# Kernel tuning notes

Measured on AMD Instinct MI355X. Metric: run time of the kernel, lower is better.

## Reference

```python
import jax, jax.numpy as jnp
import numpy as np

NUM_STEPS = 50   # global num_steps in source
SCALE = 1000     # global scale in source (fc1 out / fc2 in)
SUBTHRESH = 0.5  # HeavisideBoxcar surrogate half-width
THRESH = 1.0     # firing threshold

@jax.custom_vjp
def heaviside_boxcar(x):
    # spike = H(x); surrogate grad = boxcar of half-width SUBTHRESH
    return (x >= 0.0).astype(x.dtype)

def _hb_fwd(x):
    return heaviside_boxcar(x), x

def _hb_bwd(x, g):
    return (g * (jnp.abs(x) < SUBTHRESH).astype(g.dtype),)

heaviside_boxcar.defvjp(_hb_fwd, _hb_bwd)


def setup_inputs() -> dict:
    key = jax.random.key(0)
    k1, k2, k3 = jax.random.split(key, 3)
    B = 1024
    x = jax.random.uniform(k1, (B, 784), dtype=jnp.float32)  # pixel intensities in [0,1]
    W1 = jax.random.normal(k2, (SCALE, 784), jnp.float32) / np.sqrt(784).astype(np.float32)
    W2 = jax.random.normal(k3, (100, SCALE), jnp.float32) / np.sqrt(SCALE).astype(np.float32)
    tau_0 = jnp.array([2.0], jnp.float32)       # sigmoid(2) ~ 0.88 decay
    tau_vector = jnp.array([2.0], jnp.float32)
    acc_tau = jnp.array([2.0], jnp.float32)
    return {"x": x, "W1": W1, "W2": W2, "tau_0": tau_0,
            "tau_vector": tau_vector, "acc_tau": acc_tau}


def reference(x, W1, W2, tau_0, tau_vector, acc_tau):
    B = x.shape[0]
    # snn.spikegen.rate: per-step Bernoulli(p=x) spikes, shape [T, B, 784]
    u = jax.random.uniform(jax.random.key(42), (NUM_STEPS, B, 784), dtype=x.dtype)
    x_spk = (u < x[None]).astype(x.dtype)

    decay_0 = jax.nn.sigmoid(tau_0[0])
    decay_v = jax.nn.sigmoid(tau_vector[0])
    acc_decay = jax.nn.sigmoid(acc_tau[0])

    h1_mem = jnp.full((B, SCALE), 0.5, x.dtype)
    h1_spk = jnp.zeros((B, SCALE), x.dtype)
    h2_mem = jnp.full((B, 100), 0.5, x.dtype)
    h2_spk = jnp.zeros((B, 100), x.dtype)
    acc = jnp.zeros((B, 10), x.dtype)

    def step(carry, xt):
        h1m, h1s, h2m, h2s, acc = carry
        # pPLIF: mem = mem*decay*(1-spk) + I ; spike = H(mem - thresh)
        h1m = h1m * decay_0 * (1.0 - h1s) + xt @ W1.T
        h1s = heaviside_boxcar(h1m - THRESH)
        h2m = h2m * decay_v * (1.0 - h2s) + h1s @ W2.T
        h2s = heaviside_boxcar(h2m - THRESH)
        boost = jnp.mean(h2s.reshape(B, 10, 10), axis=2)  # AvgPool1d(10,10)
        acc = acc * acc_decay + boost                      # pPLI accumulator
        return (h1m, h1s, h2m, h2s, acc), None

    carry, _ = jax.lax.scan(step, (h1_mem, h1_spk, h2_mem, h2_spk, acc),
                            x_spk[:NUM_STEPS - 1])
    # torch loop runs under no_grad with detach(): block grads through it
    h1m, h1s, h2m, h2s, acc = jax.tree_util.tree_map(jax.lax.stop_gradient, carry)

    # final, differentiable step
    h1m = h1m * decay_0 * (1.0 - h1s) + x_spk[NUM_STEPS - 1] @ W1.T
    h1s = heaviside_boxcar(h1m - THRESH)
    h2m = h2m * decay_v * (1.0 - h2s) + h1s @ W2.T
    h2s = heaviside_boxcar(h2m - THRESH)
    boost = jnp.mean(h2s.reshape(B, 10, 10), axis=2)
    acc = acc * acc_decay + boost
    return acc
```

## Files before the change

kernel.cpp:

```cpp
#include <hip/hip_runtime.h>
#include <hip/hip_bf16.h>
#include <math.h>


#define NSTEPS 50
#define KC1 13
#define NSL 5
#define SYNC_EVERY 5

typedef __attribute__((ext_vector_type(4)))  int i32x4;
typedef __attribute__((ext_vector_type(16))) int i32x16;

#define OFF_B1     0ull
#define OFF_B2     4259840ull
#define OFF_AF     4915200ull
#define OFF_H1SC   47513600ull
#define OFF_T2     99942400ull
#define OFF_H2M    152371200ull
#define OFF_H2S    153419776ull
#define OFF_ACC    153550848ull
#define OFF_BAR    153632768ull
#define WS_END     153633280ull

#define PREP_BLOCKS 3840
#define SPK_BLOCKS 10400

__device__ __forceinline__ unsigned int rotl32(unsigned int v, int d) {
#if __has_builtin(__builtin_amdgcn_alignbit)
  return __builtin_amdgcn_alignbit(v, v, (unsigned int)(32 - d));
#else
  return (v << d) | (v >> (32 - d));
#endif
}

__device__ __forceinline__ unsigned int tf_bits(unsigned int i) {
  const unsigned int ks0 = 0u;
  const unsigned int ks1 = 42u;
  const unsigned int ks2 = 0x1BD11BDAu ^ 0u ^ 42u;
  unsigned int x0 = 0u + ks0;
  unsigned int x1 = i + ks1;
#define TF_RND(r) { x0 += x1; x1 = rotl32(x1, r); x1 ^= x0; }
  TF_RND(13) TF_RND(15) TF_RND(26) TF_RND(6)
  x0 += ks1; x1 += ks2 + 1u;
  TF_RND(17) TF_RND(29) TF_RND(16) TF_RND(24)
  x0 += ks2; x1 += ks0 + 2u;
  TF_RND(13) TF_RND(15) TF_RND(26) TF_RND(6)
  x0 += ks0; x1 += ks1 + 3u;
  TF_RND(17) TF_RND(29) TF_RND(16) TF_RND(24)
  x0 += ks1; x1 += ks2 + 4u;
  TF_RND(13) TF_RND(15) TF_RND(26) TF_RND(6)
  x0 += ks2; x1 += ks0 + 5u;
#undef TF_RND
  return x0 ^ x1;
}

__device__ __forceinline__ void spike_block(
    const float* __restrict__ x, i32x4* __restrict__ A, int gblk, int tid) {
  int g = gblk * 4 + (tid >> 6);
  int lane = tid & 63;
  int kc = g % 13;
  int r = g / 13;
  int mt = r & 63;
  int t = r >> 6;
  int b = mt * 16 + (lane & 15);
  int j0 = kc * 64 + ((lane >> 4) << 4);
  unsigned int wds[4] = {0u, 0u, 0u, 0u};
  if (j0 < 784) {
    unsigned int base = (unsigned int)(t * 1024 + b) * 784u + (unsigned int)j0;
    const float* xp = x + b * 784 + j0;
#pragma unroll
    for (int q = 0; q < 4; ++q) {
      float4 xv = *(const float4*)(xp + 4 * q);
      unsigned int K0 = (unsigned int)(int)ceilf(xv.x * 8388608.0f);
      unsigned int K1 = (unsigned int)(int)ceilf(xv.y * 8388608.0f);
      unsigned int K2 = (unsigned int)(int)ceilf(xv.z * 8388608.0f);
      unsigned int K3 = (unsigned int)(int)ceilf(xv.w * 8388608.0f);
      unsigned int w4 = 0u;
      if ((tf_bits(base + 4 * q + 0) >> 9) < K0) w4 |= 1u;
      if ((tf_bits(base + 4 * q + 1) >> 9) < K1) w4 |= 1u << 8;
      if ((tf_bits(base + 4 * q + 2) >> 9) < K2) w4 |= 1u << 16;
      if ((tf_bits(base + 4 * q + 3) >> 9) < K3) w4 |= 1u << 24;
      wds[q] = w4;
    }
  }
  i32x4 v;
  v.x = (int)wds[0]; v.y = (int)wds[1]; v.z = (int)wds[2]; v.w = (int)wds[3];
  A[(size_t)((t * 64 + mt) * 13 + kc) * 64 + lane] = v;
}

__global__ __launch_bounds__(256) void setup_kernel(
    const float* __restrict__ W1, const float* __restrict__ W2,
    signed char* __restrict__ B1, signed char* __restrict__ B2,
    const float* __restrict__ x, i32x4* __restrict__ A,
    unsigned int* __restrict__ bar) {
  if (blockIdx.x >= PREP_BLOCKS) {
    spike_block(x, A, blockIdx.x - PREP_BLOCKS, threadIdx.x);
    return;
  }
  if (blockIdx.x == 0 && threadIdx.x < 128) bar[threadIdx.x] = 0u;
  int idx = blockIdx.x * 256 + threadIdx.x;
  const int NB1 = 64 * 13 * 64 * 16;
  float w;
  signed char* dst;
  size_t stride;
  if (idx < NB1) {
    int jj = idx & 15;
    int lane = (idx >> 4) & 63;
    int kc = (idx >> 10) % 13;
    int nt = (idx >> 10) / 13;
    int k = kc * 64 + ((lane >> 4) << 4) + jj;
    int o = nt * 16 + (lane & 15);
    w = (o < 1000 && k < 784) ? W1[o * 784 + k] : 0.0f;
    dst = B1 + (size_t)(nt * 13 + kc) * 5120 + (lane << 4) + jj;
    stride = 1024;
  } else {
    int m2 = idx - NB1;
    int jj = m2 & 15;
    int lane = (m2 >> 4) & 63;
    int kc = (m2 >> 10) & 31;
    int nt = (m2 >> 10) >> 5;
    int k = kc * 32 + ((lane >> 5) << 4) + jj;
    int o = nt * 32 + (lane & 31);
    w = (o < 100 && k < 1000) ? W2[o * 1000 + k] : 0.0f;
    dst = B2 + (size_t)(nt * 32 + kc) * 1024 + (lane << 4) + jj;
    stride = 4 * 32 * 1024;
  }
  long long V = llrint((double)w * 281474976710656.0);
  signed char d = (signed char)(V & 0xFF);
  V = (V - (long long)d) >> 8;
#pragma unroll
  for (int s = 0; s < 5; ++s) {
    d = (signed char)(V & 0xFF);
    V = (V - (long long)d) >> 8;
    dst[(size_t)s * stride] = d;
  }
}

#define F1_EPI16(CP, mi, hpp, r) do {                                         \
    double td = (double)CP[4][r];                                             \
    td = td * 256.0 + (double)CP[3][r];                                       \
    td = td * 256.0 + (double)CP[2][r];                                       \
    td = td * 256.0 + (double)CP[1][r];                                       \
    td = td * 256.0 + (double)CP[0][r];                                       \
    double I = td * 0x1p-40;                                                  \
    double mm = (((spk >> (mi)) & 1u) ? 0.0 : m[mi] * alpha) + I;             \
    m[mi] = mm;                                                               \
    unsigned int sp = ((mm - 1.0) >= 0.0) ? 1u : 0u;                          \
    spk = (spk & ~(1u << (mi))) | (sp << (mi));                               \
    hpp[(r) * 16] = (signed char)sp;                                          \
  } while (0)

#define F1_STEP(WA, WB, EA, EB, DOEPI, LAST, PAR) do {                        \
    _Pragma("unroll")                                                         \
    for (int kc = 0; kc < 13; ++kc) {                                         \
      const int sl = (kc + (PAR)) & 1;                                        \
      i32x4 avA = aA[sl], avB = aB[sl];                                       \
      if (kc + 2 < 13) {                                                      \
        aA[sl] = AtA[(kc + 2) * 64];                                          \
        aB[sl] = AtB[(kc + 2) * 64];                                          \
      } else if (!(LAST)) {                                                   \
        aA[sl] = AtA[(kc + 2 - 13) * 64 + 53248];                             \
        aB[sl] = AtB[(kc + 2 - 13) * 64 + 53248];                             \
      }                                                                       \
      i32x4 q0 = bR[sl][0], q1 = bR[sl][1],                                   \
            q2 = bR[sl][2], q3 = bR[sl][3];                                   \
      i32x4 q4 = p4[kc];                                                      \
      if (kc + 2 < 13) {                                                      \
        _Pragma("unroll")                                                     \
        for (int s = 0; s < 4; ++s)                                           \
          bR[sl][s] = blsv[((kc + 2) * 4 + s) * 64 + lane];                   \
      } else {                                                                \
        _Pragma("unroll")                                                     \
        for (int s = 0; s < 4; ++s)                                           \
          bR[sl][s] = blsv[((kc + 2 - 13) * 4 + s) * 64 + lane];              \
      }                                                                       \
      if (kc == 0) {                                                          \
        WA[0] = __builtin_amdgcn_mfma_i32_16x16x64_i8(avA, q0, Z, 0, 0, 0);   \
        WB[0] = __builtin_amdgcn_mfma_i32_16x16x64_i8(avB, q0, Z, 0, 0, 0);   \
        WA[1] = __builtin_amdgcn_mfma_i32_16x16x64_i8(avA, q1, Z, 0, 0, 0);   \
        WB[1] = __builtin_amdgcn_mfma_i32_16x16x64_i8(avB, q1, Z, 0, 0, 0);   \
        WA[2] = __builtin_amdgcn_mfma_i32_16x16x64_i8(avA, q2, Z, 0, 0, 0);   \
        WB[2] = __builtin_amdgcn_mfma_i32_16x16x64_i8(avB, q2, Z, 0, 0, 0);   \
        WA[3] = __builtin_amdgcn_mfma_i32_16x16x64_i8(avA, q3, Z, 0, 0, 0);   \
        WB[3] = __builtin_amdgcn_mfma_i32_16x16x64_i8(avB, q3, Z, 0, 0, 0);   \
        WA[4] = __builtin_amdgcn_mfma_i32_16x16x64_i8(avA, q4, Z, 0, 0, 0);   \
        WB[4] = __builtin_amdgcn_mfma_i32_16x16x64_i8(avB, q4, Z, 0, 0, 0);   \
      } else {                                                                \
        WA[0] = __builtin_amdgcn_mfma_i32_16x16x64_i8(avA, q0, WA[0], 0,0,0); \
        WB[0] = __builtin_amdgcn_mfma_i32_16x16x64_i8(avB, q0, WB[0], 0,0,0); \
        WA[1] = __builtin_amdgcn_mfma_i32_16x16x64_i8(avA, q1, WA[1], 0,0,0); \
        WB[1] = __builtin_amdgcn_mfma_i32_16x16x64_i8(avB, q1, WB[1], 0,0,0); \
        WA[2] = __builtin_amdgcn_mfma_i32_16x16x64_i8(avA, q2, WA[2], 0,0,0); \
        WB[2] = __builtin_amdgcn_mfma_i32_16x16x64_i8(avB, q2, WB[2], 0,0,0); \
        WA[3] = __builtin_amdgcn_mfma_i32_16x16x64_i8(avA, q3, WA[3], 0,0,0); \
        WB[3] = __builtin_amdgcn_mfma_i32_16x16x64_i8(avB, q3, WB[3], 0,0,0); \
        WA[4] = __builtin_amdgcn_mfma_i32_16x16x64_i8(avA, q4, WA[4], 0,0,0); \
        WB[4] = __builtin_amdgcn_mfma_i32_16x16x64_i8(avB, q4, WB[4], 0,0,0); \
      }                                                                       \
      if ((DOEPI) && kc >= 1 && kc <= 4) F1_EPI16(EA, kc - 1, hpA, kc - 1);   \
      if ((DOEPI) && kc >= 5 && kc <= 8) F1_EPI16(EB, kc - 1, hpB, kc - 5);   \
    }                                                                         \
    if (DOEPI) { hpA += 1048576; hpB += 1048576; }                            \
    if (!(LAST)) { AtA += 53248; AtB += 53248; }                              \
  } while (0)

__global__ __launch_bounds__(512, 1) void fused1_kernel(
    const signed char* __restrict__ B1, const i32x4* __restrict__ Afc,
    signed char* __restrict__ h1sc, const float* __restrict__ tau0,
    unsigned int* __restrict__ bar) {
  extern __shared__ i32x4 blsv[];
  const int tid = threadIdx.x, lane = tid & 63, wv = tid >> 6;
  const int id = (int)blockIdx.x;
  const int mtg = id & 3, nt = id >> 2;
  const int mtA = mtg * 16 + wv * 2;
  const i32x4* B1v = (const i32x4*)B1;

  for (int r = tid; r < 3328; r += 512) {
    int kc = r >> 8;
    int rem = r & 255;
    blsv[r] = B1v[(size_t)nt * 4160 + (size_t)kc * 320 + rem];
  }

  i32x4 p4[13];
#pragma unroll
  for (int kc = 0; kc < 13; ++kc)
    p4[kc] = B1v[(size_t)nt * 4160 + (size_t)kc * 320 + 4 * 64 + lane];

  const double alpha = 1.0 / (1.0 + exp(-(double)tau0[0]));
  double m[8];
  unsigned int spk = 0;
#pragma unroll
  for (int r = 0; r < 8; ++r) m[r] = 0.5;

  i32x4 Z;
  Z.x = 0; Z.y = 0; Z.z = 0; Z.w = 0;
  i32x4 Ca[5], Cb[5];
  i32x4 Da[5], Db[5];

  const i32x4* AtA = Afc + (size_t)(mtA * 13) * 64 + lane;
  const i32x4* AtB = AtA + 13 * 64;
  signed char* hpA = h1sc
      + ((size_t)(nt) * 1024 + mtA * 16 + ((lane >> 4) << 2)) * 16
      + (lane & 15);
  signed char* hpB = hpA + 16 * 16;

  i32x4 aA[2], aB[2];
  aA[0] = AtA[0]; aA[1] = AtA[64];
  aB[0] = AtB[0]; aB[1] = AtB[64];

  __syncthreads();

  i32x4 bR[2][4];
#pragma unroll
  for (int kc = 0; kc < 2; ++kc)
#pragma unroll
    for (int s = 0; s < 4; ++s)
      bR[kc][s] = blsv[(kc * 4 + s) * 64 + lane];

  F1_STEP(Ca, Cb, Da, Db, 0, 0, 0);
#pragma unroll 1
  for (int tp = 0; tp < 24; ++tp) {
    F1_STEP(Da, Db, Ca, Cb, 1, 0, 1);
    F1_STEP(Ca, Cb, Da, Db, 1, 0, 0);
    if (((tp + 1) % 5) == 0) {
      __syncthreads();
      if (tid == 0) {
        int ph = (tp + 1) / 5 - 1;
        unsigned int* c = bar + (mtg << 4) + ph;
        __hip_atomic_fetch_add(c, 1u, __ATOMIC_RELAXED,
                               __HIP_MEMORY_SCOPE_AGENT);
        for (int spin = 0; spin < 20000; ++spin) {
          if (__hip_atomic_load(c, __ATOMIC_RELAXED,
                                __HIP_MEMORY_SCOPE_AGENT) >= 64u) break;
          __builtin_amdgcn_s_sleep(2);
        }
      }
      __syncthreads();
    }
  }
  F1_STEP(Da, Db, Ca, Cb, 1, 1, 1);
#pragma unroll
  for (int r = 0; r < 4; ++r) F1_EPI16(Da, r, hpA, r);
#pragma unroll
  for (int r = 0; r < 4; ++r) F1_EPI16(Db, r + 4, hpB, r);
}

__global__ __launch_bounds__(256, 3) void gemm2_kernel(
    const signed char* __restrict__ Bf, const signed char* __restrict__ h1sc,
    double* __restrict__ T2) {
  __shared__ i32x4 bls[2][NSL][64];
  int tid = threadIdx.x, lane = tid & 63, wv = tid >> 6;
  int nt = blockIdx.x & 3;
  int mg = blockIdx.x >> 2;
  int tl = mg >> 3;
  int mt = ((mg & 7) << 2) + wv;
  const i32x4* Ar = (const i32x4*)h1sc
      + ((size_t)tl * 64 + (lane >> 5)) * 1024 + mt * 32 + (lane & 31);
  const i32x4* Bp = (const i32x4*)Bf + lane;
  const bool st4 = (wv == 0);
#define B2_IDX(s, kc) ((size_t)(((s) * 4 + nt) * 32 + (kc)) * 64)

  i32x16 C[NSL];
#pragma unroll
  for (int s = 0; s < NSL; ++s)
#pragma unroll
    for (int i = 0; i < 16; ++i) C[s][i] = 0;

  i32x4 sa = Bp[B2_IDX(wv, 0)];
  i32x4 sb; if (st4) sb = Bp[B2_IDX(4, 0)];
  i32x4 a0 = Ar[0];
  i32x4 a1 = Ar[2048];
  i32x4 a2;
  bls[0][wv][lane] = sa;
  if (st4) bls[0][4][lane] = sb;
  sa = Bp[B2_IDX(wv, 1)];
  if (st4) sb = Bp[B2_IDX(4, 1)];
  __syncthreads();

  for (int kc = 0; kc < 32; ++kc) {
    const int cur = kc & 1, nxt = cur ^ 1;
    if (kc + 1 < 32) {
      bls[nxt][wv][lane] = sa;
      if (st4) bls[nxt][4][lane] = sb;
    }
    if (kc + 2 < 32) {
      sa = Bp[B2_IDX(wv, kc + 2)];
      if (st4) sb = Bp[B2_IDX(4, kc + 2)];
      a2 = Ar[(size_t)(kc + 2) * 2048];
    }
    i32x4 b0 = bls[cur][0][lane], b1 = bls[cur][1][lane], b2 = bls[cur][2][lane];
    i32x4 b3 = bls[cur][3][lane], b4 = bls[cur][4][lane];
    C[0] = __builtin_amdgcn_mfma_i32_32x32x32_i8(a0, b0, C[0], 0, 0, 0);
    C[1] = __builtin_amdgcn_mfma_i32_32x32x32_i8(a0, b1, C[1], 0, 0, 0);
    C[2] = __builtin_amdgcn_mfma_i32_32x32x32_i8(a0, b2, C[2], 0, 0, 0);
    C[3] = __builtin_amdgcn_mfma_i32_32x32x32_i8(a0, b3, C[3], 0, 0, 0);
    C[4] = __builtin_amdgcn_mfma_i32_32x32x32_i8(a0, b4, C[4], 0, 0, 0);
    a0 = a1; a1 = a2;
    __syncthreads();
  }

  int o = nt * 32 + (lane & 31);
  int rb = 4 * (lane >> 5);
#pragma unroll
  for (int r = 0; r < 16; ++r) {
    int row = (r & 3) + 8 * (r >> 2) + rb;
    int b = mt * 32 + row;
    long long T = (long long)C[4][r];
    T = (T << 8) + (long long)C[3][r];
    T = (T << 8) + (long long)C[2][r];
    T = (T << 8) + (long long)C[1][r];
    T = (T << 8) + (long long)C[0][r];
    T2[((size_t)tl * 1024 + b) * 128 + o] = (double)T * 0x1p-40;
  }
}

__global__ __launch_bounds__(256) void rec2_kernel(
    const double* __restrict__ T2, double* __restrict__ h2m_st,
    signed char* __restrict__ h2s_st, double* __restrict__ acc_st,
    const float* __restrict__ tauv, const float* __restrict__ acct,
    int t0, int C, float* __restrict__ out) {
  __shared__ signed char sp[256];
  int tid = threadIdx.x;
  int b = blockIdx.x * 2 + (tid >> 7);
  int o = tid & 127;
  double alpha = 1.0 / (1.0 + exp(-(double)tauv[0]));
  double adec  = 1.0 / (1.0 + exp(-(double)acct[0]));
  double m, s, accv = 0.0;
  bool isPool = (o < 10);
  if (t0 == 0) {
    m = 0.5; s = 0.0;
  } else {
    m = h2m_st[(size_t)b * 128 + o];
    s = (double)h2s_st[(size_t)b * 128 + o];
    if (isPool) accv = acc_st[b * 10 + o];
  }
  for (int tl = 0; tl < C; ++tl) {
    double I = T2[((size_t)tl * 1024 + b) * 128 + o];
    m = (s != 0.0 ? 0.0 : m * alpha) + I;
    bool spk = (m - 1.0) >= 0.0;
    s = spk ? 1.0 : 0.0;
    sp[tid] = spk ? 1 : 0;
    __syncthreads();
    if (isPool) {
      int base = tid & 128;
      int isum = 0;
#pragma unroll
      for (int k = 0; k < 10; ++k) isum += sp[base + o * 10 + k];
      accv = accv * adec + (double)isum / 10.0;
      if (t0 + tl == NSTEPS - 1) out[b * 10 + o] = (float)accv;
    }
    __syncthreads();
  }
  h2m_st[(size_t)b * 128 + o] = m;
  h2s_st[(size_t)b * 128 + o] = (signed char)(s != 0.0 ? 1 : 0);
  if (isPool) acc_st[b * 10 + o] = accv;
}

extern "C" void kernel_launch(void* const* d_in, const int* in_sizes, int n_in,
                              void* d_out, int out_size, void* d_ws, size_t ws_size,
                              hipStream_t stream) {
  const float* x    = (const float*)d_in[0];
  const float* W1   = (const float*)d_in[1];
  const float* W2   = (const float*)d_in[2];
  const float* tau0 = (const float*)d_in[3];
  const float* tauv = (const float*)d_in[4];
  const float* acct = (const float*)d_in[5];
  float* out = (float*)d_out;
  char*  ws  = (char*)d_ws;

  signed char* B1     = (signed char*)(ws + OFF_B1);
  signed char* B2     = (signed char*)(ws + OFF_B2);
  signed char* Af     = (signed char*)(ws + OFF_AF);
  signed char* h1sc   = (signed char*)(ws + OFF_H1SC);
  double*      T2     = (double*)(ws + OFF_T2);
  double*      h2m_st = (double*)(ws + OFF_H2M);
  signed char* h2s_st = (signed char*)(ws + OFF_H2S);
  double*      acc_st = (double*)(ws + OFF_ACC);
  unsigned int* bar   = (unsigned int*)(ws + OFF_BAR);
  i32x4*       Afv    = (i32x4*)Af;

  static bool attr_done = false;
  if (!attr_done) {
    (void)hipFuncSetAttribute((const void*)fused1_kernel,
                              hipFuncAttributeMaxDynamicSharedMemorySize,
                              53248);
    attr_done = true;
  }

  setup_kernel<<<PREP_BLOCKS + SPK_BLOCKS, 256, 0, stream>>>(
      W1, W2, B1, B2, x, Afv, bar);

  fused1_kernel<<<256, 512, 53248, stream>>>(B1, Afv, h1sc, tau0, bar);

  gemm2_kernel<<<4 * NSTEPS * 8, 256, 0, stream>>>(B2, h1sc, T2);

  rec2_kernel<<<512, 256, 0, stream>>>(
      T2, h2m_st, h2s_st, acc_st, tauv, acct, 0, NSTEPS, out);
}
```

Baseline: 406.3 us.

## Compress layer-2 intermediate to int+short and move one B1 slice to registers

The gemm2 output, previously stored as doubles, is now stored as a 32-bit low part plus a 16-bit high part of the exact integer accumulator. This cuts the bytes written and read between gemm2 and rec2 from 8 to 6 per element, and rec2 rebuilds the double itself. rec2 now prefetches the next step's value one iteration ahead and drops its chunked-restart parameters. In fused1, a fourth B1 sub-tile is held in registers (p3) instead of LDS, which shrinks shared memory and LDS reads at the cost of more register pressure.

```diff
diff --git a/kernel.cpp b/kernel.cpp
--- a/kernel.cpp
+++ b/kernel.cpp
@@ -15,12 +15,13 @@
 #define OFF_B2     4259840ull
 #define OFF_AF     4915200ull
 #define OFF_H1SC   47513600ull
-#define OFF_T2     99942400ull
-#define OFF_H2M    152371200ull
-#define OFF_H2S    153419776ull
-#define OFF_ACC    153550848ull
-#define OFF_BAR    153632768ull
-#define WS_END     153633280ull
+#define OFF_T2L    99942400ull
+#define OFF_T2H    126156800ull
+#define OFF_H2M    139264000ull
+#define OFF_H2S    140312576ull
+#define OFF_ACC    140443648ull
+#define OFF_BAR    140525568ull
+#define WS_END     140526080ull
 
 #define PREP_BLOCKS 3840
 #define SPK_BLOCKS 10400
@@ -162,17 +163,16 @@
         aA[sl] = AtA[(kc + 2 - 13) * 64 + 53248];                             \
         aB[sl] = AtB[(kc + 2 - 13) * 64 + 53248];                             \
       }                                                                       \
-      i32x4 q0 = bR[sl][0], q1 = bR[sl][1],                                   \
-            q2 = bR[sl][2], q3 = bR[sl][3];                                   \
-      i32x4 q4 = p4[kc];                                                      \
+      i32x4 q0 = bR[sl][0], q1 = bR[sl][1], q2 = bR[sl][2];                   \
+      i32x4 q3 = p3[kc], q4 = p4[kc];                                         \
       if (kc + 2 < 13) {                                                      \
         _Pragma("unroll")                                                     \
-        for (int s = 0; s < 4; ++s)                                           \
-          bR[sl][s] = blsv[((kc + 2) * 4 + s) * 64 + lane];                   \
+        for (int s = 0; s < 3; ++s)                                           \
+          bR[sl][s] = blsv[((kc + 2) * 3 + s) * 64 + lane];                   \
       } else {                                                                \
         _Pragma("unroll")                                                     \
-        for (int s = 0; s < 4; ++s)                                           \
-          bR[sl][s] = blsv[((kc + 2 - 13) * 4 + s) * 64 + lane];              \
+        for (int s = 0; s < 3; ++s)                                           \
+          bR[sl][s] = blsv[((kc + 2 - 13) * 3 + s) * 64 + lane];              \
       }                                                                       \
       if (kc == 0) {                                                          \
         WA[0] = __builtin_amdgcn_mfma_i32_16x16x64_i8(avA, q0, Z, 0, 0, 0);   \
@@ -215,16 +215,18 @@
   const int mtA = mtg * 16 + wv * 2;
   const i32x4* B1v = (const i32x4*)B1;
 
-  for (int r = tid; r < 3328; r += 512) {
-    int kc = r >> 8;
-    int rem = r & 255;
+  for (int r = tid; r < 2496; r += 512) {
+    int kc = r / 192;
+    int rem = r - kc * 192;
     blsv[r] = B1v[(size_t)nt * 4160 + (size_t)kc * 320 + rem];
   }
 
-  i32x4 p4[13];
-#pragma unroll
-  for (int kc = 0; kc < 13; ++kc)
+  i32x4 p3[13], p4[13];
+#pragma unroll
+  for (int kc = 0; kc < 13; ++kc) {
+    p3[kc] = B1v[(size_t)nt * 4160 + (size_t)kc * 320 + 3 * 64 + lane];
     p4[kc] = B1v[(size_t)nt * 4160 + (size_t)kc * 320 + 4 * 64 + lane];
+  }
 
   const double alpha = 1.0 / (1.0 + exp(-(double)tau0[0]));
   double m[8];
@@ -250,12 +252,12 @@
 
   __syncthreads();
 
-  i32x4 bR[2][4];
+  i32x4 bR[2][3];
 #pragma unroll
   for (int kc = 0; kc < 2; ++kc)
 #pragma unroll
-    for (int s = 0; s < 4; ++s)
-      bR[kc][s] = blsv[(kc * 4 + s) * 64 + lane];
+    for (int s = 0; s < 3; ++s)
+      bR[kc][s] = blsv[(kc * 3 + s) * 64 + lane];
 
   F1_STEP(Ca, Cb, Da, Db, 0, 0, 0);
 #pragma unroll 1
@@ -287,7 +289,7 @@
 
 __global__ __launch_bounds__(256, 3) void gemm2_kernel(
     const signed char* __restrict__ Bf, const signed char* __restrict__ h1sc,
-    double* __restrict__ T2) {
+    int* __restrict__ T2L, short* __restrict__ T2H) {
   __shared__ i32x4 bls[2][NSL][64];
   int tid = threadIdx.x, lane = tid & 63, wv = tid >> 6;
   int nt = blockIdx.x & 3;
@@ -350,32 +352,38 @@
     T = (T << 8) + (long long)C[2][r];
     T = (T << 8) + (long long)C[1][r];
     T = (T << 8) + (long long)C[0][r];
-    T2[((size_t)tl * 1024 + b) * 128 + o] = (double)T * 0x1p-40;
+    size_t i0 = ((size_t)tl * 1024 + b) * 128 + o;
+    T2L[i0] = (int)T;
+    T2H[i0] = (short)(T >> 32);
   }
 }
 
 __global__ __launch_bounds__(256) void rec2_kernel(
-    const double* __restrict__ T2, double* __restrict__ h2m_st,
+    const int* __restrict__ T2L, const short* __restrict__ T2H,
+    double* __restrict__ h2m_st,
     signed char* __restrict__ h2s_st, double* __restrict__ acc_st,
     const float* __restrict__ tauv, const float* __restrict__ acct,
-    int t0, int C, float* __restrict__ out) {
+    float* __restrict__ out) {
   __shared__ signed char sp[256];
   int tid = threadIdx.x;
   int b = blockIdx.x * 2 + (tid >> 7);
   int o = tid & 127;
   double alpha = 1.0 / (1.0 + exp(-(double)tauv[0]));
   double adec  = 1.0 / (1.0 + exp(-(double)acct[0]));
-  double m, s, accv = 0.0;
+  double m = 0.5, s = 0.0, accv = 0.0;
   bool isPool = (o < 10);
-  if (t0 == 0) {
-    m = 0.5; s = 0.0;
-  } else {
-    m = h2m_st[(size_t)b * 128 + o];
-    s = (double)h2s_st[(size_t)b * 128 + o];
-    if (isPool) accv = acc_st[b * 10 + o];
-  }
-  for (int tl = 0; tl < C; ++tl) {
-    double I = T2[((size_t)tl * 1024 + b) * 128 + o];
+  const int*   Lp = T2L + (size_t)b * 128 + o;
+  const short* Hp = T2H + (size_t)b * 128 + o;
+  int   Tl = Lp[0];
+  short Th = Hp[0];
+  for (int tl = 0; tl < NSTEPS; ++tl) {
+    int Tl2 = 0; short Th2 = 0;
+    if (tl + 1 < NSTEPS) {
+      Tl2 = Lp[(size_t)(tl + 1) * 131072];
+      Th2 = Hp[(size_t)(tl + 1) * 131072];
+    }
+    long long T = ((long long)Th << 32) + (long long)(unsigned int)Tl;
+    double I = (double)T * 0x1p-40;
     m = (s != 0.0 ? 0.0 : m * alpha) + I;
     bool spk = (m - 1.0) >= 0.0;
     s = spk ? 1.0 : 0.0;
@@ -387,9 +395,10 @@
 #pragma unroll
       for (int k = 0; k < 10; ++k) isum += sp[base + o * 10 + k];
       accv = accv * adec + (double)isum / 10.0;
-      if (t0 + tl == NSTEPS - 1) out[b * 10 + o] = (float)accv;
+      if (tl == NSTEPS - 1) out[b * 10 + o] = (float)accv;
     }
     __syncthreads();
+    Tl = Tl2; Th = Th2;
   }
   h2m_st[(size_t)b * 128 + o] = m;
   h2s_st[(size_t)b * 128 + o] = (signed char)(s != 0.0 ? 1 : 0);
@@ -412,7 +421,8 @@
   signed char* B2     = (signed char*)(ws + OFF_B2);
   signed char* Af     = (signed char*)(ws + OFF_AF);
   signed char* h1sc   = (signed char*)(ws + OFF_H1SC);
-  double*      T2     = (double*)(ws + OFF_T2);
+  int*         T2L    = (int*)(ws + OFF_T2L);
+  short*       T2H    = (short*)(ws + OFF_T2H);
   double*      h2m_st = (double*)(ws + OFF_H2M);
   signed char* h2s_st = (signed char*)(ws + OFF_H2S);
   double*      acc_st = (double*)(ws + OFF_ACC);
@@ -423,17 +433,17 @@
   if (!attr_done) {
     (void)hipFuncSetAttribute((const void*)fused1_kernel,
                               hipFuncAttributeMaxDynamicSharedMemorySize,
-                              53248);
+                              39936);
     attr_done = true;
   }
 
   setup_kernel<<<PREP_BLOCKS + SPK_BLOCKS, 256, 0, stream>>>(
       W1, W2, B1, B2, x, Afv, bar);
 
-  fused1_kernel<<<256, 512, 53248, stream>>>(B1, Afv, h1sc, tau0, bar);
-
-  gemm2_kernel<<<4 * NSTEPS * 8, 256, 0, stream>>>(B2, h1sc, T2);
+  fused1_kernel<<<256, 512, 39936, stream>>>(B1, Afv, h1sc, tau0, bar);
+
+  gemm2_kernel<<<4 * NSTEPS * 8, 256, 0, stream>>>(B2, h1sc, T2L, T2H);
 
   rec2_kernel<<<512, 256, 0, stream>>>(
-      T2, h2m_st, h2s_st, acc_st, tauv, acct, 0, NSTEPS, out);
-}
+      T2L, T2H, h2m_st, h2s_st, acc_st, tauv, acct, out);
+}
```

After: 648.2 us. 1.6x slower.
